# Optimization experiments

Hardware: AMD Instinct MI355X
Metric: run time of the kernel (lower is better)

## Reference

```python
import jax, jax.numpy as jnp
import numpy as np

B, L, D = 1, 1024, 1024
NL = 4            # n_layers
N = 16            # d_state
DI = 2 * D        # d_inner (expand=2)
DTR = (D + 15) // 16  # dt_rank = ceil(d_model/16) = 64
K = 4             # depthwise conv kernel size
EPS = 1e-5


def setup_inputs() -> dict:
    key = jax.random.key(0)
    ks = jax.random.split(key, 8)
    s = lambda k, shp, sc: jax.random.normal(k, shp, jnp.float32) * sc
    x = s(ks[0], (B, L, D), 1.0)
    norm_w = jnp.ones((NL, D), jnp.float32)
    in_w = s(ks[1], (NL, 2 * DI, D), D ** -0.5)          # in_proj (no bias)
    conv_w = s(ks[2], (NL, DI, K), 0.5)                   # depthwise conv1d weight
    conv_b = s(ks[3], (NL, DI), 0.02)                     # conv1d bias
    xproj_w = s(ks[4], (NL, DTR + 2 * N, DI), DI ** -0.5) # x_proj (no bias)
    dt_w = s(ks[5], (NL, DI, DTR), DTR ** -0.5)           # dt_proj weight
    dt_b = jnp.full((NL, DI), 0.1, jnp.float32)           # dt_proj bias (positive-ish delta)
    A_log = jnp.log(jnp.tile(jnp.arange(1, N + 1, dtype=jnp.float32), (NL, DI, 1)))  # [NL, DI, N]
    D_skip = jnp.ones((NL, DI), jnp.float32)
    out_w = s(ks[6], (NL, D, DI), DI ** -0.5)             # out_proj (no bias)
    return dict(x=x, norm_w=norm_w, in_w=in_w, conv_w=conv_w, conv_b=conv_b,
                xproj_w=xproj_w, dt_w=dt_w, dt_b=dt_b, A_log=A_log,
                D_skip=D_skip, out_w=out_w)


def _rmsnorm(x, w):
    return x * jax.lax.rsqrt(jnp.mean(x * x, axis=-1, keepdims=True) + EPS) * w


def _causal_depthwise_conv(u, w, b):
    # u: [B, L, DI], w: [DI, K], b: [DI]; causal (left pad K-1)
    up = jnp.pad(u, ((0, 0), (K - 1, 0), (0, 0)))
    y = b
    for k in range(K):
        y = y + up[:, k:k + L, :] * w[:, k]
    return y


def _selective_scan(dA, dBu, C):
    # dA, dBu: [B, L, DI, N]; C: [B, L, N]
    def step(h, inp):
        a, bu, c = inp
        h = a * h + bu                       # [B, DI, N]
        y = jnp.einsum('bdn,bn->bd', h, c)   # [B, DI]
        return h, y
    h0 = jnp.zeros((dA.shape[0], DI, N), dA.dtype)
    _, ys = jax.lax.scan(step, h0, (dA.transpose(1, 0, 2, 3),
                                    dBu.transpose(1, 0, 2, 3),
                                    C.transpose(1, 0, 2)))
    return ys.transpose(1, 0, 2)             # [B, L, DI]


def _mamba_block(x, p):
    norm_w, in_w, conv_w, conv_b, xproj_w, dt_w, dt_b, A_log, D_skip, out_w = p
    xn = _rmsnorm(x, norm_w)
    xz = jnp.einsum('bld,ed->ble', xn, in_w)             # [B, L, 2*DI]
    u, z = jnp.split(xz, 2, axis=-1)
    u = jax.nn.silu(_causal_depthwise_conv(u, conv_w, conv_b))
    x_dbl = jnp.einsum('bld,ed->ble', u, xproj_w)        # [B, L, DTR+2N]
    dt_r, Bt, Ct = jnp.split(x_dbl, [DTR, DTR + N], axis=-1)
    delta = jax.nn.softplus(jnp.einsum('blr,dr->bld', dt_r, dt_w) + dt_b)  # [B, L, DI]
    A = -jnp.exp(A_log)                                  # [DI, N]
    dA = jnp.exp(delta[..., None] * A)                   # [B, L, DI, N]
    dBu = delta[..., None] * Bt[:, :, None, :] * u[..., None]
    y = _selective_scan(dA, dBu, Ct) + u * D_skip        # [B, L, DI]
    y = y * jax.nn.silu(z)
    return x + jnp.einsum('ble,de->bld', y, out_w)       # residual


def reference(x, norm_w, in_w, conv_w, conv_b, xproj_w, dt_w, dt_b, A_log, D_skip, out_w):
    params = (norm_w, in_w, conv_w, conv_b, xproj_w, dt_w, dt_b, A_log, D_skip, out_w)
    out, _ = jax.lax.scan(lambda h, p: (_mamba_block(h, p), None), x, params)
    return out
```

## Files before the change

### kernel.cpp

```cpp
#include <hip/hip_runtime.h>
#include <hip/hip_bf16.h>
#include <stdint.h>

#define L 1024
#define D 1024
#define NLAYER 4
#define NSTATE 16
#define DI 2048
#define DTR 64
#define KCONV 4
#define XD 96
#define NC 64
#define CT 16
#define KSPLIT 16

typedef __attribute__((ext_vector_type(8))) short short8;
typedef __attribute__((ext_vector_type(4))) float floatx4;

__device__ __forceinline__ float siluf(float x) { return x / (1.f + __expf(-x)); }

__device__ __forceinline__ unsigned short f2bf(float x) {
    __hip_bfloat16 b = __float2bfloat16(x);
    return *reinterpret_cast<unsigned short*>(&b);
}

#ifndef __has_builtin
#define __has_builtin(x) 0
#endif
#if __has_builtin(__builtin_amdgcn_global_load_lds)
#define HAVE_GLD 1
#define GLD(gp, lp) __builtin_amdgcn_global_load_lds(                                  \
    (const __attribute__((address_space(1))) void*)(gp),                               \
    (__attribute__((address_space(3))) void*)(lp), 16, 0, 0)
#endif

#define N_IN4  1048576
#define N_XP4  49152
#define N_DT4  32768
#define N_OUT4 524288
#define N_CVT4 (N_IN4 + N_XP4 + N_DT4 + N_OUT4)

__global__ __launch_bounds__(256) void cvt_all_kernel(
    const float* __restrict__ in_w, const float* __restrict__ xp_w,
    const float* __restrict__ dt_w, const float* __restrict__ out_w,
    __hip_bfloat16* __restrict__ in_bf, __hip_bfloat16* __restrict__ xp_bf,
    __hip_bfloat16* __restrict__ dt_bf, __hip_bfloat16* __restrict__ out_bf) {
    int gi = blockIdx.x * 256 + threadIdx.x;
    if (gi >= NLAYER * N_CVT4) return;
    int layer = gi / N_CVT4;
    int i = gi - layer * N_CVT4;
    const float* src;
    __hip_bfloat16* dst;
    int off;
    if (i < N_IN4) {
        src = in_w + (size_t)layer * 4096 * 1024;
        dst = in_bf + (size_t)layer * 4096 * 1024; off = i;
    } else if (i < N_IN4 + N_XP4) {
        src = xp_w + (size_t)layer * 96 * 2048;
        dst = xp_bf + (size_t)layer * 128 * 2048; off = i - N_IN4;
    } else if (i < N_IN4 + N_XP4 + N_DT4) {
        src = dt_w + (size_t)layer * 2048 * 64;
        dst = dt_bf + (size_t)layer * 2048 * 64; off = i - N_IN4 - N_XP4;
    } else {
        src = out_w + (size_t)layer * 1024 * 2048;
        dst = out_bf + (size_t)layer * 1024 * 2048; off = i - N_IN4 - N_XP4 - N_DT4;
    }
    float4 v = ((const float4*)src)[off];
    ushort4 o;
    o.x = f2bf(v.x); o.y = f2bf(v.y); o.z = f2bf(v.z); o.w = f2bf(v.w);
    ((ushort4*)dst)[off] = o;
}

__global__ __launch_bounds__(256) void rmsnorm_kernel(const float* __restrict__ x,
                                                      const float* __restrict__ w,
                                                      __hip_bfloat16* __restrict__ out) {
    int row = blockIdx.x;
    const float* xr = x + (size_t)row * D;
    float v[4];
    float s = 0.f;
#pragma unroll
    for (int i = 0; i < 4; ++i) {
        v[i] = xr[threadIdx.x + i * 256];
        s += v[i] * v[i];
    }
#pragma unroll
    for (int off = 32; off > 0; off >>= 1) s += __shfl_xor(s, off, 64);
    __shared__ float red[4];
    int wave = threadIdx.x >> 6;
    if ((threadIdx.x & 63) == 0) red[wave] = s;
    __syncthreads();
    float tot = red[0] + red[1] + red[2] + red[3];
    float inv = rsqrtf(tot * (1.f / D) + 1e-5f);
#pragma unroll
    for (int i = 0; i < 4; ++i) {
        int c = threadIdx.x + i * 256;
        out[(size_t)row * D + c] = __float2bfloat16(v[i] * inv * w[c]);
    }
}

#define BK 32

template <int TN, int EPI>
__global__ __launch_bounds__(256, 2) void gemm_mfma(
    const __hip_bfloat16* __restrict__ A, int lda,
    const __hip_bfloat16* __restrict__ B, int ldb,
    float* __restrict__ C, int ldc, int Nvalid,
    int kchunk, long zstride,
    const float* __restrict__ bias, const float* __restrict__ resid) {
    constexpr int NF = TN / 32;
    constexpr int WCOLS = TN / 2;
    __shared__ __align__(16) __hip_bfloat16 As[128 * BK];
    __shared__ __align__(16) __hip_bfloat16 Bs[TN * BK];
    int tid = threadIdx.x;
    int wave = tid >> 6, lane = tid & 63;
    int m0 = blockIdx.y * 128, n0 = blockIdx.x * TN;
    int k_lo = blockIdx.z * kchunk;
    int k_hi = k_lo + kchunk;
    C += (long)blockIdx.z * zstride;
    int wr = wave >> 1, wc = wave & 1;
    int srow = lane >> 2, scol = (lane & 3) * 8;
    int q = lane >> 4, r = lane & 15;

    floatx4 acc[4][NF] = {};

    const __hip_bfloat16* gA0 = A + (long)(m0 + wave * 32 + srow) * lda + scol;
    const __hip_bfloat16* gA1 = gA0 + (long)16 * lda;
    __hip_bfloat16* lA0 = As + (wave * 32) * BK;
    __hip_bfloat16* lA1 = As + (wave * 32 + 16) * BK;
    const __hip_bfloat16* gB0;
    const __hip_bfloat16* gB1 = nullptr;
    __hip_bfloat16* lB0;
    __hip_bfloat16* lB1 = nullptr;
    if (TN == 128) {
        gB0 = B + (long)(n0 + wave * 32 + srow) * ldb + scol;
        gB1 = gB0 + (long)16 * ldb;
        lB0 = Bs + (wave * 32) * BK;
        lB1 = Bs + (wave * 32 + 16) * BK;
    } else {
        gB0 = B + (long)(n0 + wave * 16 + srow) * ldb + scol;
        lB0 = Bs + (wave * 16) * BK;
    }

    for (int k0 = k_lo; k0 < k_hi; k0 += BK) {
#ifdef HAVE_GLD
        GLD(gA0 + k0, lA0);
        GLD(gA1 + k0, lA1);
        GLD(gB0 + k0, lB0);
        if (TN == 128) GLD(gB1 + k0, lB1);
#else
        *(short8*)(lA0 + lane * 8) = *(const short8*)(gA0 + k0 - scol + (lane & 3) * 8);
        *(short8*)(lA1 + lane * 8) = *(const short8*)(gA1 + k0 - scol + (lane & 3) * 8);
        *(short8*)(lB0 + lane * 8) = *(const short8*)(gB0 + k0 - scol + (lane & 3) * 8);
        if (TN == 128) *(short8*)(lB1 + lane * 8) = *(const short8*)(gB1 + k0 - scol + (lane & 3) * 8);
#endif
        __syncthreads();
        const short* Ap = (const short*)As;
        const short* Bp = (const short*)Bs;
        short8 af[4], bfr[NF];
#pragma unroll
        for (int i = 0; i < 4; ++i)
            af[i] = *(const short8*)(Ap + (wr * 64 + i * 16 + r) * BK + q * 8);
#pragma unroll
        for (int j = 0; j < NF; ++j)
            bfr[j] = *(const short8*)(Bp + (wc * WCOLS + j * 16 + r) * BK + q * 8);
#pragma unroll
        for (int i = 0; i < 4; ++i)
#pragma unroll
            for (int j = 0; j < NF; ++j)
                acc[i][j] = __builtin_amdgcn_mfma_f32_16x16x32_bf16(af[i], bfr[j], acc[i][j], 0, 0, 0);
        __syncthreads();
    }

#pragma unroll
    for (int i = 0; i < 4; ++i) {
        int mrow = m0 + wr * 64 + i * 16 + q * 4;
#pragma unroll
        for (int j = 0; j < NF; ++j) {
            int ncol = n0 + wc * WCOLS + j * 16 + r;
            if (ncol < Nvalid) {
#pragma unroll
                for (int rr = 0; rr < 4; ++rr) {
                    float v = acc[i][j][rr];
                    int m = mrow + rr;
                    if (EPI == 1) {
                        v += bias[ncol];
                        v = v > 20.f ? v : log1pf(__expf(v));
                    } else if (EPI == 2) {
                        v += resid[(long)m * ldc + ncol];
                    }
                    C[(long)m * ldc + ncol] = v;
                }
            }
        }
    }
}

__global__ __launch_bounds__(256) void conv_silu_kernel(const float* __restrict__ xz,
                                                        const float* __restrict__ cw,
                                                        const float* __restrict__ cb,
                                                        __hip_bfloat16* __restrict__ u) {
    int idx = blockIdx.x * 256 + threadIdx.x;
    int d = idx & (DI - 1);
    int t = idx >> 11;
    float acc = cb[d];
#pragma unroll
    for (int k = 0; k < KCONV; ++k) {
        int tk = t - (KCONV - 1) + k;
        if (tk >= 0) acc += xz[(size_t)tk * (2 * DI) + d] * cw[d * KCONV + k];
    }
    u[idx] = __float2bfloat16(siluf(acc));
}

__global__ __launch_bounds__(256) void xdbl_reduce_kernel(const float* __restrict__ part,
                                                          float* __restrict__ xdbl,
                                                          __hip_bfloat16* __restrict__ xdbl_bf) {
    int i = blockIdx.x * 256 + threadIdx.x;
    float s = 0.f;
#pragma unroll
    for (int sp = 0; sp < KSPLIT; ++sp) s += part[(long)sp * L * XD + i];
    xdbl[i] = s;
    xdbl_bf[i] = __float2bfloat16(s);
}

__global__ __launch_bounds__(256) void scanA_kernel(const float* __restrict__ delta,
                                                    const __hip_bfloat16* __restrict__ u,
                                                    const float* __restrict__ xdbl,
                                                    const float* __restrict__ Alog,
                                                    float* __restrict__ Ach,
                                                    float* __restrict__ Bch) {
    int d = blockIdx.x * 256 + threadIdx.x;
    int c = blockIdx.y;
    __shared__ __align__(16) float Bsh[CT * NSTATE];
    int tt0 = threadIdx.x >> 4, c0 = threadIdx.x & 15;
    Bsh[threadIdx.x] = xdbl[(size_t)(c * CT + tt0) * XD + DTR + c0];
    __syncthreads();

    float aval[NSTATE];
    const float4* Al4 = (const float4*)(Alog + (size_t)d * NSTATE);
#pragma unroll
    for (int n4 = 0; n4 < 4; ++n4) {
        float4 t = Al4[n4];
        aval[n4 * 4 + 0] = -__expf(t.x);
        aval[n4 * 4 + 1] = -__expf(t.y);
        aval[n4 * 4 + 2] = -__expf(t.z);
        aval[n4 * 4 + 3] = -__expf(t.w);
    }
    float h[NSTATE], ap[NSTATE];
#pragma unroll
    for (int n = 0; n < NSTATE; ++n) { h[n] = 0.f; ap[n] = 1.f; }

    for (int tt = 0; tt < CT; ++tt) {
        int t = c * CT + tt;
        float dl = delta[(size_t)t * DI + d];
        float uu = __bfloat162float(u[(size_t)t * DI + d]);
        float du = dl * uu;
        const float4* Bv = (const float4*)(Bsh + tt * NSTATE);
#pragma unroll
        for (int n4 = 0; n4 < 4; ++n4) {
            float4 b = Bv[n4];
            float bb[4] = {b.x, b.y, b.z, b.w};
#pragma unroll
            for (int k = 0; k < 4; ++k) {
                int n = n4 * 4 + k;
                float a = __expf(dl * aval[n]);
                h[n] = a * h[n] + du * bb[k];
                ap[n] *= a;
            }
        }
    }
    float4* Ao = (float4*)(Ach + ((size_t)c * DI + d) * NSTATE);
    float4* Bo = (float4*)(Bch + ((size_t)c * DI + d) * NSTATE);
#pragma unroll
    for (int n4 = 0; n4 < 4; ++n4) {
        Ao[n4] = make_float4(ap[n4 * 4], ap[n4 * 4 + 1], ap[n4 * 4 + 2], ap[n4 * 4 + 3]);
        Bo[n4] = make_float4(h[n4 * 4], h[n4 * 4 + 1], h[n4 * 4 + 2], h[n4 * 4 + 3]);
    }
}

__global__ __launch_bounds__(256) void scanB_kernel(float* __restrict__ Ach,
                                                    const float* __restrict__ Bch) {
    long i = blockIdx.x * 256 + threadIdx.x;
    const long S = (long)DI * NSTATE;
    float h = 0.f;
    for (int c = 0; c < NC; ++c) {
        float a = Ach[c * S + i];
        float b = Bch[c * S + i];
        Ach[c * S + i] = h;
        h = a * h + b;
    }
}

__global__ __launch_bounds__(256) void scanC_kernel(const float* __restrict__ delta,
                                                    const __hip_bfloat16* __restrict__ u,
                                                    const float* __restrict__ xdbl,
                                                    const float* __restrict__ Alog,
                                                    const float* __restrict__ Hin,
                                                    const float* __restrict__ xz,
                                                    const float* __restrict__ Dskip,
                                                    __hip_bfloat16* __restrict__ yg) {
    int d = blockIdx.x * 256 + threadIdx.x;
    int c = blockIdx.y;
    __shared__ __align__(16) float Bsh[CT * NSTATE];
    __shared__ __align__(16) float Csh[CT * NSTATE];
    int tt0 = threadIdx.x >> 4, c0 = threadIdx.x & 15;
    Bsh[threadIdx.x] = xdbl[(size_t)(c * CT + tt0) * XD + DTR + c0];
    Csh[threadIdx.x] = xdbl[(size_t)(c * CT + tt0) * XD + DTR + NSTATE + c0];
    __syncthreads();

    float aval[NSTATE];
    const float4* Al4 = (const float4*)(Alog + (size_t)d * NSTATE);
#pragma unroll
    for (int n4 = 0; n4 < 4; ++n4) {
        float4 t = Al4[n4];
        aval[n4 * 4 + 0] = -__expf(t.x);
        aval[n4 * 4 + 1] = -__expf(t.y);
        aval[n4 * 4 + 2] = -__expf(t.z);
        aval[n4 * 4 + 3] = -__expf(t.w);
    }
    float h[NSTATE];
    const float4* Hi = (const float4*)(Hin + ((size_t)c * DI + d) * NSTATE);
#pragma unroll
    for (int n4 = 0; n4 < 4; ++n4) {
        float4 t = Hi[n4];
        h[n4 * 4 + 0] = t.x; h[n4 * 4 + 1] = t.y; h[n4 * 4 + 2] = t.z; h[n4 * 4 + 3] = t.w;
    }
    float dsk = Dskip[d];

    for (int tt = 0; tt < CT; ++tt) {
        int t = c * CT + tt;
        float dl = delta[(size_t)t * DI + d];
        float uu = __bfloat162float(u[(size_t)t * DI + d]);
        float du = dl * uu;
        const float4* Bv = (const float4*)(Bsh + tt * NSTATE);
        const float4* Cv = (const float4*)(Csh + tt * NSTATE);
        float y = 0.f;
#pragma unroll
        for (int n4 = 0; n4 < 4; ++n4) {
            float4 b = Bv[n4];
            float4 cc = Cv[n4];
            float bb[4] = {b.x, b.y, b.z, b.w};
            float cv[4] = {cc.x, cc.y, cc.z, cc.w};
#pragma unroll
            for (int k = 0; k < 4; ++k) {
                int n = n4 * 4 + k;
                float a = __expf(dl * aval[n]);
                h[n] = a * h[n] + du * bb[k];
                y += h[n] * cv[k];
            }
        }
        float z = xz[(size_t)t * (2 * DI) + DI + d];
        yg[(size_t)t * DI + d] = __float2bfloat16((y + uu * dsk) * siluf(z));
    }
}

extern "C" void kernel_launch(void* const* d_in, const int* in_sizes, int n_in,
                              void* d_out, int out_size, void* d_ws, size_t ws_size,
                              hipStream_t stream) {
    const float* x      = (const float*)d_in[0];
    const float* norm_w = (const float*)d_in[1];
    const float* in_w   = (const float*)d_in[2];
    const float* conv_w = (const float*)d_in[3];
    const float* conv_b = (const float*)d_in[4];
    const float* xproj_w= (const float*)d_in[5];
    const float* dt_w   = (const float*)d_in[6];
    const float* dt_b   = (const float*)d_in[7];
    const float* A_log  = (const float*)d_in[8];
    const float* D_skip = (const float*)d_in[9];
    const float* out_w  = (const float*)d_in[10];
    float* out = (float*)d_out;

    uint8_t* wp = (uint8_t*)d_ws;
    auto alloc = [&](size_t bytes) {
        uint8_t* p = wp;
        wp += (bytes + 255) & ~(size_t)255;
        return p;
    };
    __hip_bfloat16* w_in_bf  = (__hip_bfloat16*)alloc((size_t)NLAYER * 4096 * 1024 * 2);
    __hip_bfloat16* w_xp_bf  = (__hip_bfloat16*)alloc((size_t)NLAYER * 128 * 2048 * 2);
    __hip_bfloat16* w_dt_bf  = (__hip_bfloat16*)alloc((size_t)NLAYER * 2048 * 64 * 2);
    __hip_bfloat16* w_out_bf = (__hip_bfloat16*)alloc((size_t)NLAYER * 1024 * 2048 * 2);
    __hip_bfloat16* xn_bf    = (__hip_bfloat16*)alloc((size_t)L * D * 2);
    float*          xz       = (float*)alloc((size_t)L * 2 * DI * 4);
    __hip_bfloat16* u_bf     = (__hip_bfloat16*)alloc((size_t)L * DI * 2);
    float*          xdbl     = (float*)alloc((size_t)L * XD * 4);
    __hip_bfloat16* xdbl_bf  = (__hip_bfloat16*)alloc((size_t)L * XD * 2);
    float*          part     = (float*)alloc((size_t)KSPLIT * L * XD * 4);
    float*          delta    = (float*)alloc((size_t)L * DI * 4);
    __hip_bfloat16* yg_bf    = (__hip_bfloat16*)alloc((size_t)L * DI * 2);
    float*          Ach      = (float*)alloc((size_t)NC * DI * NSTATE * 4);
    float*          Bch      = (float*)alloc((size_t)NC * DI * NSTATE * 4);

    cvt_all_kernel<<<(NLAYER * N_CVT4 + 255) / 256, 256, 0, stream>>>(
        in_w, xproj_w, dt_w, out_w, w_in_bf, w_xp_bf, w_dt_bf, w_out_bf);

    for (int l = 0; l < NLAYER; ++l) {
        const float* xin = (l == 0) ? x : out;
        const __hip_bfloat16* wi = w_in_bf + (size_t)l * 4096 * 1024;
        const __hip_bfloat16* wx = w_xp_bf + (size_t)l * 128 * 2048;
        const __hip_bfloat16* wd = w_dt_bf + (size_t)l * 2048 * 64;
        const __hip_bfloat16* wo = w_out_bf + (size_t)l * 1024 * 2048;

        rmsnorm_kernel<<<L, 256, 0, stream>>>(xin, norm_w + (size_t)l * D, xn_bf);

        gemm_mfma<128, 0><<<dim3(4096 / 128, L / 128, 1), 256, 0, stream>>>(
            xn_bf, D, wi, D, xz, 4096, 4096, D, 0, nullptr, nullptr);

        conv_silu_kernel<<<L * DI / 256, 256, 0, stream>>>(
            xz, conv_w + (size_t)l * DI * KCONV, conv_b + (size_t)l * DI, u_bf);

        gemm_mfma<128, 0><<<dim3(1, L / 128, KSPLIT), 256, 0, stream>>>(
            u_bf, DI, wx, DI, part, XD, XD, DI / KSPLIT, (long)L * XD, nullptr, nullptr);
        xdbl_reduce_kernel<<<(L * XD) / 256, 256, 0, stream>>>(part, xdbl, xdbl_bf);

        gemm_mfma<128, 1><<<dim3(2048 / 128, L / 128, 1), 256, 0, stream>>>(
            xdbl_bf, XD, wd, DTR, delta, DI, DI, DTR, 0,
            dt_b + (size_t)l * DI, nullptr);

        scanA_kernel<<<dim3(DI / 256, NC), 256, 0, stream>>>(
            delta, u_bf, xdbl, A_log + (size_t)l * DI * NSTATE, Ach, Bch);
        scanB_kernel<<<(DI * NSTATE) / 256, 256, 0, stream>>>(Ach, Bch);
        scanC_kernel<<<dim3(DI / 256, NC), 256, 0, stream>>>(
            delta, u_bf, xdbl, A_log + (size_t)l * DI * NSTATE, Ach, xz,
            D_skip + (size_t)l * DI, yg_bf);

        gemm_mfma<64, 2><<<dim3(1024 / 64, L / 128, 1), 256, 0, stream>>>(
            yg_bf, DI, wo, DI, out, D, D, DI, 0, nullptr, xin);
    }
}
```

Measured before the change: 729.2 us.

## Double-buffer GEMM LDS tiles, shrink tile widths, and widen weight conversion

The MFMA GEMM now keeps two LDS buffers and issues the next k-slice's global-to-LDS loads before computing the current one, which removes one barrier per iteration and overlaps loads with math. The in_proj, x_proj and dt_proj GEMMs switch to 64-column tiles so more blocks run, and x_proj's split-K drops from 16 to 8. The weight conversion kernel now handles 16 floats per thread with 128-bit stores. LDS use doubles, which may lower occupancy. The x_proj weight buffer is padded to 128 rows, so the 2x64 grid only reads allocated memory.

```diff
diff --git a/kernel.cpp b/kernel.cpp
--- a/kernel.cpp
+++ b/kernel.cpp
@@ -12,16 +12,17 @@
 #define XD 96
 #define NC 64
 #define CT 16
-#define KSPLIT 16
+#define KSPLIT 8
 
 typedef __attribute__((ext_vector_type(8))) short short8;
 typedef __attribute__((ext_vector_type(4))) float floatx4;
 
 __device__ __forceinline__ float siluf(float x) { return x / (1.f + __expf(-x)); }
 
-__device__ __forceinline__ unsigned short f2bf(float x) {
-    __hip_bfloat16 b = __float2bfloat16(x);
-    return *reinterpret_cast<unsigned short*>(&b);
+__device__ __forceinline__ unsigned int f2bf2(float lo, float hi) {
+    __hip_bfloat16 a = __float2bfloat16(lo), b = __float2bfloat16(hi);
+    return (unsigned int)*reinterpret_cast<unsigned short*>(&a) |
+           ((unsigned int)*reinterpret_cast<unsigned short*>(&b) << 16);
 }
 
 #ifndef __has_builtin
@@ -39,6 +40,7 @@
 #define N_DT4  32768
 #define N_OUT4 524288
 #define N_CVT4 (N_IN4 + N_XP4 + N_DT4 + N_OUT4)
+#define CVT_THREADS (NLAYER * N_CVT4 / 4)
 
 __global__ __launch_bounds__(256) void cvt_all_kernel(
     const float* __restrict__ in_w, const float* __restrict__ xp_w,
@@ -46,9 +48,9 @@
     __hip_bfloat16* __restrict__ in_bf, __hip_bfloat16* __restrict__ xp_bf,
     __hip_bfloat16* __restrict__ dt_bf, __hip_bfloat16* __restrict__ out_bf) {
     int gi = blockIdx.x * 256 + threadIdx.x;
-    if (gi >= NLAYER * N_CVT4) return;
-    int layer = gi / N_CVT4;
-    int i = gi - layer * N_CVT4;
+    if (gi >= CVT_THREADS) return;
+    int layer = gi / (N_CVT4 / 4);
+    int i = (gi - layer * (N_CVT4 / 4)) * 4;
     const float* src;
     __hip_bfloat16* dst;
     int off;
@@ -65,10 +67,17 @@
         src = out_w + (size_t)layer * 1024 * 2048;
         dst = out_bf + (size_t)layer * 1024 * 2048; off = i - N_IN4 - N_XP4 - N_DT4;
     }
-    float4 v = ((const float4*)src)[off];
-    ushort4 o;
-    o.x = f2bf(v.x); o.y = f2bf(v.y); o.z = f2bf(v.z); o.w = f2bf(v.w);
-    ((ushort4*)dst)[off] = o;
+    const float4* s4 = (const float4*)src + off;
+    unsigned int o[8];
+#pragma unroll
+    for (int j = 0; j < 4; ++j) {
+        float4 v = s4[j];
+        o[j * 2 + 0] = f2bf2(v.x, v.y);
+        o[j * 2 + 1] = f2bf2(v.z, v.w);
+    }
+    uint4* dp = (uint4*)((unsigned short*)dst + (size_t)off * 4);
+    dp[0] = make_uint4(o[0], o[1], o[2], o[3]);
+    dp[1] = make_uint4(o[4], o[5], o[6], o[7]);
 }
 
 __global__ __launch_bounds__(256) void rmsnorm_kernel(const float* __restrict__ x,
@@ -109,8 +118,8 @@
     const float* __restrict__ bias, const float* __restrict__ resid) {
     constexpr int NF = TN / 32;
     constexpr int WCOLS = TN / 2;
-    __shared__ __align__(16) __hip_bfloat16 As[128 * BK];
-    __shared__ __align__(16) __hip_bfloat16 Bs[TN * BK];
+    __shared__ __align__(16) __hip_bfloat16 As[2][128 * BK];
+    __shared__ __align__(16) __hip_bfloat16 Bs[2][TN * BK];
     int tid = threadIdx.x;
     int wave = tid >> 6, lane = tid & 63;
     int m0 = blockIdx.y * 128, n0 = blockIdx.x * TN;
@@ -125,37 +134,36 @@
 
     const __hip_bfloat16* gA0 = A + (long)(m0 + wave * 32 + srow) * lda + scol;
     const __hip_bfloat16* gA1 = gA0 + (long)16 * lda;
-    __hip_bfloat16* lA0 = As + (wave * 32) * BK;
-    __hip_bfloat16* lA1 = As + (wave * 32 + 16) * BK;
     const __hip_bfloat16* gB0;
     const __hip_bfloat16* gB1 = nullptr;
-    __hip_bfloat16* lB0;
-    __hip_bfloat16* lB1 = nullptr;
     if (TN == 128) {
         gB0 = B + (long)(n0 + wave * 32 + srow) * ldb + scol;
         gB1 = gB0 + (long)16 * ldb;
-        lB0 = Bs + (wave * 32) * BK;
-        lB1 = Bs + (wave * 32 + 16) * BK;
     } else {
         gB0 = B + (long)(n0 + wave * 16 + srow) * ldb + scol;
-        lB0 = Bs + (wave * 16) * BK;
-    }
-
+    }
+
+    auto stage = [&](int k0, int p) {
+#ifdef HAVE_GLD
+        GLD(gA0 + k0, &As[p][(wave * 32) * BK]);
+        GLD(gA1 + k0, &As[p][(wave * 32 + 16) * BK]);
+        GLD(gB0 + k0, &Bs[p][(wave * (TN == 128 ? 32 : 16)) * BK]);
+        if (TN == 128) GLD(gB1 + k0, &Bs[p][(wave * 32 + 16) * BK]);
+#else
+        *(short8*)(&As[p][(wave * 32) * BK] + lane * 8) = *(const short8*)(gA0 + k0);
+        *(short8*)(&As[p][(wave * 32 + 16) * BK] + lane * 8) = *(const short8*)(gA1 + k0);
+        *(short8*)(&Bs[p][(wave * (TN == 128 ? 32 : 16)) * BK] + lane * 8) = *(const short8*)(gB0 + k0);
+        if (TN == 128) *(short8*)(&Bs[p][(wave * 32 + 16) * BK] + lane * 8) = *(const short8*)(gB1 + k0);
+#endif
+    };
+
+    stage(k_lo, 0);
+    int p = 0;
     for (int k0 = k_lo; k0 < k_hi; k0 += BK) {
-#ifdef HAVE_GLD
-        GLD(gA0 + k0, lA0);
-        GLD(gA1 + k0, lA1);
-        GLD(gB0 + k0, lB0);
-        if (TN == 128) GLD(gB1 + k0, lB1);
-#else
-        *(short8*)(lA0 + lane * 8) = *(const short8*)(gA0 + k0 - scol + (lane & 3) * 8);
-        *(short8*)(lA1 + lane * 8) = *(const short8*)(gA1 + k0 - scol + (lane & 3) * 8);
-        *(short8*)(lB0 + lane * 8) = *(const short8*)(gB0 + k0 - scol + (lane & 3) * 8);
-        if (TN == 128) *(short8*)(lB1 + lane * 8) = *(const short8*)(gB1 + k0 - scol + (lane & 3) * 8);
-#endif
         __syncthreads();
-        const short* Ap = (const short*)As;
-        const short* Bp = (const short*)Bs;
+        if (k0 + BK < k_hi) stage(k0 + BK, p ^ 1);
+        const short* Ap = (const short*)As[p];
+        const short* Bp = (const short*)Bs[p];
         short8 af[4], bfr[NF];
 #pragma unroll
         for (int i = 0; i < 4; ++i)
@@ -168,7 +176,7 @@
 #pragma unroll
             for (int j = 0; j < NF; ++j)
                 acc[i][j] = __builtin_amdgcn_mfma_f32_16x16x32_bf16(af[i], bfr[j], acc[i][j], 0, 0, 0);
-        __syncthreads();
+        p ^= 1;
     }
 
 #pragma unroll
@@ -390,7 +398,7 @@
     float*          Ach      = (float*)alloc((size_t)NC * DI * NSTATE * 4);
     float*          Bch      = (float*)alloc((size_t)NC * DI * NSTATE * 4);
 
-    cvt_all_kernel<<<(NLAYER * N_CVT4 + 255) / 256, 256, 0, stream>>>(
+    cvt_all_kernel<<<(CVT_THREADS + 255) / 256, 256, 0, stream>>>(
         in_w, xproj_w, dt_w, out_w, w_in_bf, w_xp_bf, w_dt_bf, w_out_bf);
 
     for (int l = 0; l < NLAYER; ++l) {
@@ -402,17 +410,17 @@
 
         rmsnorm_kernel<<<L, 256, 0, stream>>>(xin, norm_w + (size_t)l * D, xn_bf);
 
-        gemm_mfma<128, 0><<<dim3(4096 / 128, L / 128, 1), 256, 0, stream>>>(
+        gemm_mfma<64, 0><<<dim3(4096 / 64, L / 128, 1), 256, 0, stream>>>(
             xn_bf, D, wi, D, xz, 4096, 4096, D, 0, nullptr, nullptr);
 
         conv_silu_kernel<<<L * DI / 256, 256, 0, stream>>>(
             xz, conv_w + (size_t)l * DI * KCONV, conv_b + (size_t)l * DI, u_bf);
 
-        gemm_mfma<128, 0><<<dim3(1, L / 128, KSPLIT), 256, 0, stream>>>(
+        gemm_mfma<64, 0><<<dim3(2, L / 128, KSPLIT), 256, 0, stream>>>(
             u_bf, DI, wx, DI, part, XD, XD, DI / KSPLIT, (long)L * XD, nullptr, nullptr);
         xdbl_reduce_kernel<<<(L * XD) / 256, 256, 0, stream>>>(part, xdbl, xdbl_bf);
 
-        gemm_mfma<128, 1><<<dim3(2048 / 128, L / 128, 1), 256, 0, stream>>>(
+        gemm_mfma<64, 1><<<dim3(2048 / 64, L / 128, 1), 256, 0, stream>>>(
             xdbl_bf, XD, wd, DTR, delta, DI, DI, DTR, 0,
             dt_b + (size_t)l * DI, nullptr);
 
```

Result: faster. 669.3 us (-8.2%).
